# Optimization experiments

Measured on AMD Instinct MI355X. Metric: run time of the kernel, lower is better.

The kernel has to match this reference:

```python
import jax, jax.numpy as jnp
import numpy as np

B, L1, L2, D = 16, 512, 512, 512
H, INNER = 8, 1024
HD = INNER // H  # 128

def _glorot(key, shape):
    fan_in, fan_out = shape[-2], shape[-1]
    lim = jnp.sqrt(6.0 / (fan_in + fan_out))
    return jax.random.uniform(key, shape, jnp.float32, -lim, lim)

def setup_inputs() -> dict:
    key = jax.random.key(0)
    ks = jax.random.split(key, 8)
    return {
        "primary": jax.random.normal(ks[0], (B, L1, D), jnp.float32),
        "secondary": jax.random.normal(ks[1], (B, L2, D), jnp.float32),
        "primary_mask": jnp.ones((B, L1), jnp.float32),
        "secondary_mask": jnp.ones((B, L2), jnp.float32),
        "W_aff": _glorot(ks[2], (H, D, D)),          # per-head bilinear affinity weights
        "W_p": _glorot(ks[3], (D, INNER)),            # linear_primary (no bias)
        "W_s": _glorot(ks[4], (D, INNER)),            # linear_secondary (no bias)
        "W_fp": _glorot(ks[5], (D + HD, D)),          # ffn_primary
        "b_fp": jnp.zeros((D,), jnp.float32),
        "W_fs": _glorot(ks[6], (D + HD, D)),          # ffn_secondary
        "b_fs": jnp.zeros((D,), jnp.float32),
    }

def reference(primary, secondary, primary_mask, secondary_mask,
              W_aff, W_p, W_s, W_fp, b_fp, W_fs, b_fs):
    b, l1, d = primary.shape
    l2 = secondary.shape[1]
    h = W_aff.shape[0]
    hd = W_p.shape[1] // h
    # affinity mask: (B, 1, L1, L2)
    mask = (primary_mask[:, :, None] * secondary_mask[:, None, :])[:, None, :, :]
    # multi-head bilinear affinity: tanh(P Wk S^T) -> (B, H, L1, L2)
    aff = jnp.tanh(jnp.einsum('bie,hef,bjf->bhij', primary, W_aff, secondary)) * mask
    # project + split heads -> (B, H, L, hd)
    pp = (primary @ W_p).reshape(b, l1, h, hd).transpose(0, 2, 1, 3)
    ps = (secondary @ W_s).reshape(b, l2, h, hd).transpose(0, 2, 1, 3)
    # weighted sums (ReLU activation)
    wp = jax.nn.relu(jnp.einsum('bhij,bhid->bhjd', aff, pp))  # (B, H, L2, hd)
    ws = jax.nn.relu(jnp.einsum('bhij,bhjd->bhid', aff, ps))  # (B, H, L1, hd)
    # GlobalMaxPool1D applied to (L, H, hd) per sample => max over heads
    pool_p = wp.max(axis=1)  # (B, L2, hd)
    pool_s = ws.max(axis=1)  # (B, L1, hd)
    out_p = jax.nn.relu(jnp.concatenate([primary, pool_s], -1) @ W_fp + b_fp)
    out_s = jax.nn.relu(jnp.concatenate([secondary, pool_p], -1) @ W_fs + b_fs)
    return out_p, out_s
```

## Files before the change

### kernel.cpp

```cpp
#include <hip/hip_runtime.h>
#include <hip/hip_bf16.h>

typedef short short8 __attribute__((ext_vector_type(8)));
typedef float f32x16 __attribute__((ext_vector_type(16)));

#define BM 128
#define BN 128

typedef const __attribute__((address_space(1))) void gas_t;
typedef __attribute__((address_space(3))) void las_t;

__device__ __forceinline__ unsigned short f2bf(float f) {
  unsigned int u = __float_as_uint(f);
  u += 0x7FFFu + ((u >> 16) & 1u);
  return (unsigned short)(u >> 16);
}

__device__ __forceinline__ float fast_tanh(float x) {
  x = fminf(fmaxf(x, -10.f), 10.f);
  float t = __builtin_amdgcn_exp2f(x * 2.8853900817779268f);
  return 1.f - 2.f * __builtin_amdgcn_rcpf(t + 1.f);
}

struct GemmP {
  const unsigned short* A;
  const unsigned short* Bm;
  void* C;
  const float* A2f;
  const unsigned short* A_b;
  const unsigned short* Bm_b;
  void* C_b;
  const float* A2f_b;
  const float* mask_p;
  const float* mask_s;
  const float* bias;
  const float* bias_b;
  long long sAb, sAh, sBb, sBh, sCb, sCh;
  int lda, lda2, ldb, ldc, M, N, K, Hh, kSplit, zSplit, nbx, nby;
};

template <int TA, int EPI>
__device__ __forceinline__ void gemm_body(const GemmP& p, int bx, int by, int bz, char* smem_) {
  constexpr int PA = (TA == 0) ? 32 : 40;
  constexpr int HSA = (TA == 0) ? 4096 : 5120;
  unsigned short* As = (unsigned short*)smem_;
  unsigned short* Bs = (unsigned short*)(smem_ + 2 * HSA * 2);

  int z = bz;
  const unsigned short* Abase = p.A;
  const unsigned short* Bbase = p.Bm;
  void* Cvp = p.C;
  const float* A2f = p.A2f;
  const float* bias = p.bias;
  if (p.zSplit && z >= p.zSplit) {
    z -= p.zSplit;
    Abase = p.A_b; Bbase = p.Bm_b; Cvp = p.C_b; A2f = p.A2f_b; bias = p.bias_b;
  }
  const int zb = z / p.Hh, zh = z % p.Hh;
  const unsigned short* A = Abase + (size_t)zb * p.sAb + (size_t)zh * p.sAh;
  const unsigned short* B = Bbase + (size_t)zb * p.sBb + (size_t)zh * p.sBh;
  const int m0 = bx * BM, n0 = by * BN;
  const int tid = threadIdx.x;
  const int wid = tid >> 6, lane = tid & 63;
  const int wm = (wid >> 1) * 64, wn = (wid & 1) * 64;
  const int lrow = lane & 31;
  const int lk8 = (lane >> 5) * 8;

  f32x16 acc[2][2] = {};

  const int dm = tid >> 2, dkg = tid & 3;

  auto mfma_block = [&]() {
#pragma unroll
    for (int h = 0; h < 2; ++h)
#pragma unroll
      for (int kc = 0; kc < 2; ++kc) {
        short8 af[2], bfv[2];
#pragma unroll
        for (int mt = 0; mt < 2; ++mt)
          af[mt] = *(const short8*)&As[h * HSA + (wm + mt * 32 + lrow) * PA + kc * 16 + lk8];
#pragma unroll
        for (int nt = 0; nt < 2; ++nt)
          bfv[nt] = *(const short8*)&Bs[h * 4096 + (wn + nt * 32 + lrow) * 32 + kc * 16 + lk8];
#pragma unroll
        for (int mt = 0; mt < 2; ++mt)
#pragma unroll
          for (int nt = 0; nt < 2; ++nt)
            acc[mt][nt] = __builtin_amdgcn_mfma_f32_32x32x16_bf16(af[mt], bfv[nt], acc[mt][nt], 0, 0, 0);
      }
  };
  auto stage_b = [&](int k0) {
#pragma unroll
    for (int h = 0; h < 2; ++h)
#pragma unroll
      for (int q = 0; q < 2; ++q) {
        const unsigned short* src = B + (size_t)(n0 + q * 64 + dm) * p.ldb + (k0 + h * 32 + dkg * 8);
        __builtin_amdgcn_global_load_lds((gas_t*)src,
                                         (las_t*)&Bs[h * 4096 + q * 2048 + wid * 512],
                                         16, 0, 0);
      }
  };

  const int nIter = p.K >> 6;
  const int nIter1 = p.kSplit ? (p.kSplit >> 6) : nIter;

  for (int it = 0; it < nIter1; ++it) {
    const int k0 = it << 6;
    if (TA == 0) {
#pragma unroll
      for (int h = 0; h < 2; ++h)
#pragma unroll
        for (int q = 0; q < 2; ++q) {
          const unsigned short* src = A + (size_t)(m0 + q * 64 + dm) * p.lda + (k0 + h * 32 + dkg * 8);
          __builtin_amdgcn_global_load_lds((gas_t*)src,
                                           (las_t*)&As[h * HSA + q * 2048 + wid * 512],
                                           16, 0, 0);
        }
    } else {
      const int kk = tid & 31, mg = (tid >> 5) << 4;
#pragma unroll
      for (int h = 0; h < 2; ++h) {
        const unsigned short* src = A + (size_t)(k0 + h * 32 + kk) * p.lda + (m0 + mg);
        uint4 v0 = *(const uint4*)src;
        uint4 v1 = *(const uint4*)(src + 8);
        unsigned short tmp[16];
        *(uint4*)&tmp[0] = v0;
        *(uint4*)&tmp[8] = v1;
#pragma unroll
        for (int j = 0; j < 16; ++j) As[h * HSA + (mg + j) * PA + kk] = tmp[j];
      }
    }
    stage_b(k0);
    __syncthreads();
    mfma_block();
    __syncthreads();
  }

  if (TA == 0 && p.kSplit) {
    for (int it = nIter1; it < nIter; ++it) {
      const int k0 = it << 6;
#pragma unroll
      for (int h = 0; h < 2; ++h) {
        const int ko = k0 + h * 32 - p.kSplit;
#pragma unroll
        for (int q = 0; q < 2; ++q) {
          const float* src = A2f + (size_t)(m0 + q * 64 + dm) * p.lda2 + (ko + dkg * 8);
          float4 v0 = *(const float4*)src;
          float4 v1 = *(const float4*)(src + 4);
          __attribute__((aligned(16))) unsigned short t[8];
          t[0] = f2bf(v0.x); t[1] = f2bf(v0.y); t[2] = f2bf(v0.z); t[3] = f2bf(v0.w);
          t[4] = f2bf(v1.x); t[5] = f2bf(v1.y); t[6] = f2bf(v1.z); t[7] = f2bf(v1.w);
          *(uint4*)&As[h * HSA + (q * 64 + dm) * 32 + dkg * 8] = *(const uint4*)t;
        }
      }
      stage_b(k0);
      __syncthreads();
      mfma_block();
      __syncthreads();
    }
  }

  unsigned short* Cu = (unsigned short*)Cvp + (size_t)zb * p.sCb + (size_t)zh * p.sCh;
  float* Cf = (float*)Cvp + (size_t)zb * p.sCb + (size_t)zh * p.sCh;

  const int rbase = 4 * (lane >> 5);

  float mp[2][16], ms[2];
  if constexpr (EPI == 1) {
#pragma unroll
    for (int mt = 0; mt < 2; ++mt)
#pragma unroll
      for (int reg = 0; reg < 16; ++reg) {
        const int rl = (reg & 3) + 8 * (reg >> 2) + rbase;
        mp[mt][reg] = p.mask_p[(size_t)zb * p.M + (m0 + wm + mt * 32 + rl)];
      }
#pragma unroll
    for (int nt = 0; nt < 2; ++nt)
      ms[nt] = p.mask_s[(size_t)zb * p.N + (n0 + wn + nt * 32 + lrow)];
  }
  if constexpr (EPI == 3) {
#pragma unroll
    for (int nt = 0; nt < 2; ++nt)
      ms[nt] = bias[n0 + wn + nt * 32 + lrow];
  }

#pragma unroll
  for (int mt = 0; mt < 2; ++mt) {
#pragma unroll
    for (int nt = 0; nt < 2; ++nt) {
      f32x16 a = acc[mt][nt];
#pragma unroll
      for (int reg = 0; reg < 16; ++reg) {
        const int rl = (reg & 3) + 8 * (reg >> 2) + rbase;
        const int grow = m0 + wm + mt * 32 + rl;
        const int gcol = n0 + wn + nt * 32 + lrow;
        const size_t idx = (size_t)grow * p.ldc + gcol;
        const float v = a[reg];
        if constexpr (EPI == 0) {
          Cu[idx] = f2bf(v);
        } else if constexpr (EPI == 1) {
          Cu[idx] = f2bf(fast_tanh(v) * (mp[mt][reg] * ms[nt]));
        } else if constexpr (EPI == 2) {
          atomicMax((int*)Cf + idx, __float_as_int(fmaxf(v, 0.f)));
        } else {
          Cf[idx] = fmaxf(v + ms[nt], 0.f);
        }
      }
    }
  }
}

template <int TA, int EPI>
__global__ __launch_bounds__(256) void gemm_k(GemmP p) {
  extern __shared__ char smem[];
  gemm_body<TA, EPI>(p, blockIdx.x, blockIdx.y, blockIdx.z, smem);
}

template <int TA1, int EPI1, int TA2, int EPI2>
__global__ __launch_bounds__(256) void gemm_pair_k(GemmP a, GemmP b, int nA) {
  extern __shared__ char smem[];
  int bid = blockIdx.x;
  if (bid < nA) {
    const int per = a.nbx * a.nby;
    const int z = bid / per, r = bid % per;
    gemm_body<TA1, EPI1>(a, r % a.nbx, r / a.nbx, z, smem);
  } else {
    bid -= nA;
    const int per = b.nbx * b.nby;
    const int z = bid / per, r = bid % per;
    gemm_body<TA2, EPI2>(b, r % b.nbx, r / b.nbx, z, smem);
  }
}

__device__ __forceinline__ void trans_body(const float* src, unsigned short* dst,
                                           int R, int C, int bx, int by, float (*tile)[33]) {
  const int r0 = by * 32, c0 = bx * 32;
  const int tx = threadIdx.x & 31, ty = threadIdx.x >> 5;
#pragma unroll
  for (int j = 0; j < 4; ++j)
    tile[ty + j * 8][tx] = src[(size_t)(r0 + ty + j * 8) * C + (c0 + tx)];
  __syncthreads();
#pragma unroll
  for (int j = 0; j < 4; ++j)
    dst[(size_t)(c0 + ty + j * 8) * R + (r0 + tx)] = f2bf(tile[tx][ty + j * 8]);
}

__global__ __launch_bounds__(256) void prep_k(const float* P, const float* S,
                                              unsigned short* Pbf, unsigned short* Sbf,
                                              const float* W_aff, unsigned short* WaT,
                                              const float* W_p, unsigned short* WpT,
                                              const float* W_s, unsigned short* WsT,
                                              const float* W_fp, unsigned short* WfpT,
                                              const float* W_fs, unsigned short* WfsT,
                                              float* poolz) {
  __shared__ float tile[32][33];
  const int bid = blockIdx.x;
  if (bid < 8192) {
    const int n4 = 1048576;
    int i = bid * 256 + threadIdx.x;
    const float4* s = (const float4*)P;
    ushort4* d = (ushort4*)Pbf;
    if (i >= n4) { i -= n4; s = (const float4*)S; d = (ushort4*)Sbf; }
    float4 v = s[i];
    ushort4 o;
    o.x = f2bf(v.x); o.y = f2bf(v.y); o.z = f2bf(v.z); o.w = f2bf(v.w);
    d[i] = o;
  } else if (bid < 10240) {
    const int l = bid - 8192;
    const int z = l >> 8, r = l & 255;
    trans_body(W_aff + (size_t)z * 262144, WaT + (size_t)z * 262144, 512, 512,
               r & 15, r >> 4, tile);
  } else if (bid < 11264) {
    const int l = bid - 10240;
    const int z = l >> 9, r = l & 511;
    trans_body(z ? W_s : W_p, z ? WsT : WpT, 512, 1024, r & 31, r >> 5, tile);
  } else if (bid < 11904) {
    const int l = bid - 11264;
    const int z = l / 320, r = l % 320;
    trans_body(z ? W_fs : W_fp, z ? WfsT : WfpT, 640, 512, r & 15, r >> 4, tile);
  } else {
    const int i = (bid - 11904) * 256 + threadIdx.x;
    ((float4*)poolz)[i] = float4{0.f, 0.f, 0.f, 0.f};
  }
}

extern "C" void kernel_launch(void* const* d_in, const int* in_sizes, int n_in,
                              void* d_out, int out_size, void* d_ws, size_t ws_size,
                              hipStream_t stream) {
  (void)in_sizes; (void)n_in; (void)out_size; (void)ws_size;
  const float* primary   = (const float*)d_in[0];
  const float* secondary = (const float*)d_in[1];
  const float* pmask     = (const float*)d_in[2];
  const float* smask     = (const float*)d_in[3];
  const float* W_aff     = (const float*)d_in[4];
  const float* W_p       = (const float*)d_in[5];
  const float* W_s       = (const float*)d_in[6];
  const float* W_fp      = (const float*)d_in[7];
  const float* b_fp      = (const float*)d_in[8];
  const float* W_fs      = (const float*)d_in[9];
  const float* b_fs      = (const float*)d_in[10];

  constexpr int Bb = 16, L = 512, Dd = 512, Hh = 8, HDd = 128, INNER = 1024, CAT = 640;
  constexpr int NT = Hh * Dd;
  constexpr long long LD = (long long)L * Dd;
  constexpr long long LL = (long long)L * L;

  char* base = (char*)d_ws;
  size_t off = 0;
  auto alloc = [&](size_t bytes) -> void* {
    void* r = base + off;
    off += (bytes + 255) & ~(size_t)255;
    return r;
  };

  unsigned short* Pbf   = (unsigned short*)alloc((size_t)Bb * L * Dd * 2);
  unsigned short* Sbf   = (unsigned short*)alloc((size_t)Bb * L * Dd * 2);
  unsigned short* WaT   = (unsigned short*)alloc((size_t)NT * Dd * 2);
  unsigned short* WpT   = (unsigned short*)alloc((size_t)INNER * Dd * 2);
  unsigned short* WsT   = (unsigned short*)alloc((size_t)INNER * Dd * 2);
  unsigned short* WfpT  = (unsigned short*)alloc((size_t)Dd * CAT * 2);
  unsigned short* WfsT  = (unsigned short*)alloc((size_t)Dd * CAT * 2);
  unsigned short* psT   = (unsigned short*)alloc((size_t)Bb * INNER * L * 2);
  unsigned short* ppT   = (unsigned short*)alloc((size_t)Bb * INNER * L * 2);
  unsigned short* Tbuf  = (unsigned short*)alloc((size_t)Bb * L * NT * 2);
  unsigned short* affb  = (unsigned short*)alloc((size_t)Bb * Hh * L * L * 2);
  float* pool_p = (float*)alloc((size_t)Bb * L * HDd * 4);
  float* pool_s = (float*)alloc((size_t)Bb * L * HDd * 4);

  prep_k<<<dim3(13952), dim3(256), 0, stream>>>(primary, secondary, Pbf, Sbf,
                                                W_aff, WaT, W_p, WpT, W_s, WsT,
                                                W_fp, WfpT, W_fs, WfsT, pool_p);

  {
    GemmP a{};
    a.A = Pbf; a.lda = Dd;
    a.Bm = WaT; a.ldb = Dd;
    a.C = Tbuf; a.ldc = NT;
    a.M = Bb * L; a.N = NT; a.K = Dd; a.Hh = 1; a.nbx = 64; a.nby = 32;

    GemmP b{};
    b.A = WsT; b.lda = Dd; b.sAb = 0;
    b.Bm = Sbf; b.ldb = Dd; b.sBb = LD;
    b.C = psT; b.ldc = L; b.sCb = (long long)INNER * L;
    b.A_b = WpT; b.Bm_b = Pbf; b.C_b = ppT;
    b.M = INNER; b.N = L; b.K = Dd; b.Hh = 1; b.zSplit = Bb; b.nbx = 8; b.nby = 4;

    gemm_pair_k<0, 0, 0, 0><<<dim3(2048 + 1024), dim3(256), 32768, stream>>>(a, b, 2048);
  }

  {
    GemmP g{};
    g.A = Tbuf; g.lda = NT; g.sAb = (long long)L * NT; g.sAh = Dd;
    g.Bm = Sbf; g.ldb = Dd; g.sBb = LD; g.sBh = 0;
    g.C = affb; g.ldc = L; g.sCb = (long long)Hh * LL; g.sCh = LL;
    g.mask_p = pmask; g.mask_s = smask;
    g.M = L; g.N = L; g.K = Dd; g.Hh = Hh;
    gemm_k<0, 1><<<dim3(4, 4, Bb * Hh), dim3(256), 32768, stream>>>(g);
  }

  {
    GemmP g4{};
    g4.A = affb; g4.lda = L; g4.sAb = (long long)Hh * LL; g4.sAh = LL;
    g4.Bm = psT; g4.ldb = L; g4.sBb = (long long)INNER * L; g4.sBh = (long long)HDd * L;
    g4.C = pool_s; g4.ldc = HDd; g4.sCb = (long long)L * HDd; g4.sCh = 0;
    g4.M = L; g4.N = HDd; g4.K = L; g4.Hh = Hh; g4.nbx = 4; g4.nby = 1;

    GemmP g5 = g4;
    g5.Bm = ppT;
    g5.C = pool_p;

    gemm_pair_k<0, 2, 1, 2><<<dim3(512 + 512), dim3(256), 36864, stream>>>(g4, g5, 512);
  }

  {
    GemmP g{};
    g.A = Pbf; g.lda = Dd;
    g.A2f = pool_s; g.lda2 = HDd; g.kSplit = Dd;
    g.Bm = WfpT; g.ldb = CAT;
    g.C = d_out; g.ldc = Dd;
    g.bias = b_fp;
    g.A_b = Sbf; g.A2f_b = pool_p; g.Bm_b = WfsT;
    g.C_b = (float*)d_out + (size_t)Bb * L * Dd;
    g.bias_b = b_fs;
    g.M = Bb * L; g.N = Dd; g.K = CAT; g.Hh = 1; g.zSplit = 1;
    gemm_k<0, 3><<<dim3(64, 4, 2), dim3(256), 32768, stream>>>(g);
  }
}
```

Measured before the change: 333.9 us.

## Add 256x128 triple-buffered direct-to-LDS GEMM for projection and affinity GEMMs

Introduces a new 512-thread GEMM kernel with a 256x128 output tile. It streams tiles straight from global memory into LDS through a three-slot ring buffer using global_load_lds, uses explicit vmcnt waits and barriers, and raises wave priority around the MFMA bursts. The fused projection GEMMs and the tanh/mask affinity GEMM now use this kernel, with grids resized to match. The goal is more operand reuse per block and better overlap of memory loads with MFMA work. The cost is 144KB of LDS per block, which allows only one block per CU and makes hand-placed waitcnt correctness fragile.

```diff
diff --git a/kernel.cpp b/kernel.cpp
--- a/kernel.cpp
+++ b/kernel.cpp
@@ -3,6 +3,7 @@
 
 typedef short short8 __attribute__((ext_vector_type(8)));
 typedef float f32x16 __attribute__((ext_vector_type(16)));
+typedef float f32x4 __attribute__((ext_vector_type(4)));
 
 #define BM 128
 #define BN 128
@@ -229,6 +230,168 @@
     const int per = b.nbx * b.nby;
     const int z = bid / per, r = bid % per;
     gemm_body<TA2, EPI2>(b, r % b.nbx, r / b.nbx, z, smem);
+  }
+}
+
+#define VMCNT6() asm volatile("s_waitcnt vmcnt(6)" ::: "memory")
+#define VMCNT0() asm volatile("s_waitcnt vmcnt(0)" ::: "memory")
+
+template <int EPI>
+__device__ __forceinline__ void gemm8_body(const GemmP& p, int bx, int by, int bz, char* smem_) {
+  int z = bz;
+  const unsigned short* Abase = p.A;
+  const unsigned short* Bbase = p.Bm;
+  void* Cvp = p.C;
+  if (p.zSplit && z >= p.zSplit) {
+    z -= p.zSplit;
+    Abase = p.A_b; Bbase = p.Bm_b; Cvp = p.C_b;
+  }
+  const int zb = z / p.Hh, zh = z % p.Hh;
+  const unsigned short* A = Abase + (size_t)zb * p.sAb + (size_t)zh * p.sAh;
+  const unsigned short* B = Bbase + (size_t)zb * p.sBb + (size_t)zh * p.sBh;
+  const int m0 = bx * 256, n0 = by * 128;
+  const int tid = threadIdx.x;
+  const int wid = tid >> 6, lane = tid & 63;
+  const int wm = wid >> 1, wn = wid & 1;
+  const int lrow = lane & 15, lhi = lane >> 4;
+
+  unsigned short* lds_u = (unsigned short*)smem_;
+
+  const int rr = tid >> 3;
+  const int cc = ((tid & 7) * 8) ^ ((rr & 7) << 3);
+
+  const int laneA0 = (wm * 64 + lrow) * 128 + ((lhi * 16) ^ ((lrow & 7) << 4));
+  const int laneB0 = (wn * 64 + lrow) * 128 + ((lhi * 16) ^ ((lrow & 7) << 4));
+
+  f32x4 acc[4][4] = {};
+
+  auto stageA = [&](int t, int slot) {
+    const int k0 = t << 6;
+    const unsigned short* s0 = A + (size_t)(m0 + rr) * p.lda + k0 + cc;
+#pragma unroll
+    for (int s = 0; s < 4; ++s)
+      __builtin_amdgcn_global_load_lds((gas_t*)(s0 + (size_t)s * 64 * p.lda),
+                                       (las_t*)(lds_u + slot * 24576 + s * 4096 + wid * 512),
+                                       16, 0, 0);
+  };
+  auto stageB = [&](int t, int slot) {
+    const int k0 = t << 6;
+    const unsigned short* s0 = B + (size_t)(n0 + rr) * p.ldb + k0 + cc;
+#pragma unroll
+    for (int s = 0; s < 2; ++s)
+      __builtin_amdgcn_global_load_lds((gas_t*)(s0 + (size_t)s * 64 * p.ldb),
+                                       (las_t*)(lds_u + slot * 24576 + 16384 + s * 4096 + wid * 512),
+                                       16, 0, 0);
+  };
+
+  const int nt = p.K >> 6;
+
+  stageA(0, 0); stageB(0, 0);
+  stageA(1, 1); stageB(1, 1);
+  VMCNT6();
+  __builtin_amdgcn_s_barrier();
+  __builtin_amdgcn_sched_barrier(0);
+
+  int slot = 0;
+  for (int t = 0; t < nt; ++t) {
+    const int s1 = (slot == 2) ? 0 : slot + 1;
+    const int s2 = (s1 == 2) ? 0 : s1 + 1;
+    const char* baseA0 = smem_ + slot * 49152 + laneA0;
+    const char* baseA1 = smem_ + slot * 49152 + (laneA0 ^ 64);
+    const char* baseB0 = smem_ + slot * 49152 + 32768 + laneB0;
+    const char* baseB1 = smem_ + slot * 49152 + 32768 + (laneB0 ^ 64);
+    short8 af[4], bv[4];
+
+#pragma unroll
+    for (int fm = 0; fm < 4; ++fm) af[fm] = *(const short8*)(baseA0 + fm * 2048);
+#pragma unroll
+    for (int fn = 0; fn < 4; ++fn) bv[fn] = *(const short8*)(baseB0 + fn * 2048);
+    if (t + 2 < nt) stageA(t + 2, s2);
+    __builtin_amdgcn_s_barrier();
+    __builtin_amdgcn_sched_barrier(0);
+    __builtin_amdgcn_s_setprio(1);
+#pragma unroll
+    for (int fm = 0; fm < 4; ++fm)
+#pragma unroll
+      for (int fn = 0; fn < 4; ++fn)
+        acc[fm][fn] = __builtin_amdgcn_mfma_f32_16x16x32_bf16(af[fm], bv[fn], acc[fm][fn], 0, 0, 0);
+    __builtin_amdgcn_s_setprio(0);
+    __builtin_amdgcn_s_barrier();
+    __builtin_amdgcn_sched_barrier(0);
+
+#pragma unroll
+    for (int fm = 0; fm < 4; ++fm) af[fm] = *(const short8*)(baseA1 + fm * 2048);
+#pragma unroll
+    for (int fn = 0; fn < 4; ++fn) bv[fn] = *(const short8*)(baseB1 + fn * 2048);
+    if (t + 2 < nt) stageB(t + 2, s2);
+    __builtin_amdgcn_s_barrier();
+    __builtin_amdgcn_sched_barrier(0);
+    __builtin_amdgcn_s_setprio(1);
+#pragma unroll
+    for (int fm = 0; fm < 4; ++fm)
+#pragma unroll
+      for (int fn = 0; fn < 4; ++fn)
+        acc[fm][fn] = __builtin_amdgcn_mfma_f32_16x16x32_bf16(af[fm], bv[fn], acc[fm][fn], 0, 0, 0);
+    __builtin_amdgcn_s_setprio(0);
+    __builtin_amdgcn_sched_barrier(0);
+
+    if (t + 1 < nt) {
+      if (t + 2 < nt) VMCNT6(); else VMCNT0();
+      __builtin_amdgcn_s_barrier();
+      __builtin_amdgcn_sched_barrier(0);
+    }
+    slot = s1;
+  }
+
+  unsigned short* Cu = (unsigned short*)Cvp + (size_t)zb * p.sCb + (size_t)zh * p.sCh;
+
+  float mp[4][4], ms[4];
+  if constexpr (EPI == 1) {
+#pragma unroll
+    for (int fm = 0; fm < 4; ++fm)
+#pragma unroll
+      for (int reg = 0; reg < 4; ++reg)
+        mp[fm][reg] = p.mask_p[(size_t)zb * p.M + (m0 + wm * 64 + fm * 16 + lhi * 4 + reg)];
+#pragma unroll
+    for (int fn = 0; fn < 4; ++fn)
+      ms[fn] = p.mask_s[(size_t)zb * p.N + (n0 + wn * 64 + fn * 16 + lrow)];
+  }
+
+#pragma unroll
+  for (int fm = 0; fm < 4; ++fm)
+#pragma unroll
+    for (int fn = 0; fn < 4; ++fn) {
+      f32x4 a = acc[fm][fn];
+      const int gcol = n0 + wn * 64 + fn * 16 + lrow;
+#pragma unroll
+      for (int reg = 0; reg < 4; ++reg) {
+        const int grow = m0 + wm * 64 + fm * 16 + lhi * 4 + reg;
+        const size_t idx = (size_t)grow * p.ldc + gcol;
+        if constexpr (EPI == 0) Cu[idx] = f2bf(a[reg]);
+        else                    Cu[idx] = f2bf(fast_tanh(a[reg]) * (mp[fm][reg] * ms[fn]));
+      }
+    }
+}
+
+template <int EPI>
+__global__ __launch_bounds__(512, 2) void gemm8_k(GemmP p) {
+  extern __shared__ char smem[];
+  gemm8_body<EPI>(p, blockIdx.x, blockIdx.y, blockIdx.z, smem);
+}
+
+template <int E1, int E2>
+__global__ __launch_bounds__(512, 2) void gemm8_pair_k(GemmP a, GemmP b, int nA) {
+  extern __shared__ char smem[];
+  int bid = blockIdx.x;
+  if (bid < nA) {
+    const int per = a.nbx * a.nby;
+    const int z = bid / per, r = bid % per;
+    gemm8_body<E1>(a, r % a.nbx, r / a.nbx, z, smem);
+  } else {
+    bid -= nA;
+    const int per = b.nbx * b.nby;
+    const int z = bid / per, r = bid % per;
+    gemm8_body<E2>(b, r % b.nbx, r / b.nbx, z, smem);
   }
 }
 
@@ -305,6 +468,15 @@
   constexpr long long LD = (long long)L * Dd;
   constexpr long long LL = (long long)L * L;
 
+  static bool s_attr = [] {
+    hipFuncSetAttribute(reinterpret_cast<const void*>(&gemm8_pair_k<0, 0>),
+                        hipFuncAttributeMaxDynamicSharedMemorySize, 147456);
+    hipFuncSetAttribute(reinterpret_cast<const void*>(&gemm8_k<1>),
+                        hipFuncAttributeMaxDynamicSharedMemorySize, 147456);
+    return true;
+  }();
+  (void)s_attr;
+
   char* base = (char*)d_ws;
   size_t off = 0;
   auto alloc = [&](size_t bytes) -> void* {
@@ -336,16 +508,16 @@
     a.A = Pbf; a.lda = Dd;
     a.Bm = WaT; a.ldb = Dd;
     a.C = Tbuf; a.ldc = NT;
-    a.M = Bb * L; a.N = NT; a.K = Dd; a.Hh = 1; a.nbx = 64; a.nby = 32;
+    a.M = Bb * L; a.N = NT; a.K = Dd; a.Hh = 1; a.nbx = 32; a.nby = 32;
 
     GemmP b{};
     b.A = WsT; b.lda = Dd; b.sAb = 0;
     b.Bm = Sbf; b.ldb = Dd; b.sBb = LD;
     b.C = psT; b.ldc = L; b.sCb = (long long)INNER * L;
     b.A_b = WpT; b.Bm_b = Pbf; b.C_b = ppT;
-    b.M = INNER; b.N = L; b.K = Dd; b.Hh = 1; b.zSplit = Bb; b.nbx = 8; b.nby = 4;
-
-    gemm_pair_k<0, 0, 0, 0><<<dim3(2048 + 1024), dim3(256), 32768, stream>>>(a, b, 2048);
+    b.M = INNER; b.N = L; b.K = Dd; b.Hh = 1; b.zSplit = Bb; b.nbx = 4; b.nby = 4;
+
+    gemm8_pair_k<0, 0><<<dim3(1024 + 512), dim3(512), 147456, stream>>>(a, b, 1024);
   }
 
   {
@@ -355,7 +527,7 @@
     g.C = affb; g.ldc = L; g.sCb = (long long)Hh * LL; g.sCh = LL;
     g.mask_p = pmask; g.mask_s = smask;
     g.M = L; g.N = L; g.K = Dd; g.Hh = Hh;
-    gemm_k<0, 1><<<dim3(4, 4, Bb * Hh), dim3(256), 32768, stream>>>(g);
+    gemm8_k<1><<<dim3(2, 4, Bb * Hh), dim3(512), 147456, stream>>>(g);
   }
 
   {
```

New measurement: 339.6 us. About the same (+1.7%).
